# Kernel tuning notes

Hardware: AMD Instinct MI355X
Metric: run time of the kernel (lower is better)

Reference implementation:

```python
import jax, jax.numpy as jnp
import numpy as np

B, S, H = 2, 2048, 4096
NH, NKV, HD = 32, 8, 128
NEG = -1e9


def _rotary(x, cos, sin):
    # x: [b, s, h, hd]; cos/sin: [b, s, hd//2] -> broadcast over heads
    x = x.reshape(*x.shape[:-1], HD // 2, 2)
    x0, x1 = x[..., 0], x[..., 1]
    c = cos[:, :, None, :]
    s = sin[:, :, None, :]
    out = jnp.stack([x0 * c - x1 * s, x0 * s + x1 * c], axis=-1)
    return out.reshape(*out.shape[:-2], HD)


def setup_inputs() -> dict:
    key = jax.random.key(0)
    ks = jax.random.split(key, 7)
    x = jax.random.normal(ks[0], (B, S, H), dtype=jnp.float32)
    # rotary angles: standard llama freqs
    inv = 1.0 / (10000.0 ** (np.arange(0, HD, 2, dtype=np.float32) / HD))
    t = np.arange(S, dtype=np.float32)
    ang = np.outer(t, inv)  # [S, HD//2]
    freqs_cos = jnp.broadcast_to(jnp.asarray(np.cos(ang)), (B, S, HD // 2))
    freqs_sin = jnp.broadcast_to(jnp.asarray(np.sin(ang)), (B, S, HD // 2))
    sc = 0.02
    wq = jax.random.normal(ks[1], (NH * HD, H), dtype=jnp.float32) * sc
    wk = jax.random.normal(ks[2], (NKV * HD, H), dtype=jnp.float32) * sc
    wv = jax.random.normal(ks[3], (NKV * HD, H), dtype=jnp.float32) * sc
    wo = jax.random.normal(ks[4], (H, NH * HD), dtype=jnp.float32) * sc
    return {"x": x, "freqs_cos": freqs_cos, "freqs_sin": freqs_sin,
            "wq": wq, "wk": wk, "wv": wv, "wo": wo}


def reference(x, freqs_cos, freqs_sin, wq, wk, wv, wo):
    b, s, _ = x.shape
    xq = (x @ wq.T).reshape(b, s, NH, HD)
    xk = (x @ wk.T).reshape(b, s, NKV, HD)
    xv = (x @ wv.T).reshape(b, s, NKV, HD)
    xq = _rotary(xq, freqs_cos, freqs_sin)
    xk = _rotary(xk, freqs_cos, freqs_sin)
    # -> [b, heads, s, hd]
    xq = xq.transpose(0, 2, 1, 3)
    xk = xk.transpose(0, 2, 1, 3)
    xv = xv.transpose(0, 2, 1, 3)
    # prefill cache.update returns the freshly written keys/values
    n_rep = NH // NKV
    keys = jnp.repeat(xk, n_rep, axis=1)    # repeat_kv
    values = jnp.repeat(xv, n_rep, axis=1)
    scores = jnp.einsum('bhqd,bhkd->bhqk', xq, keys) / jnp.sqrt(jnp.float32(HD))
    mask = jnp.where(jnp.tril(jnp.ones((s, s), dtype=bool)), 0.0, NEG)
    scores = scores + mask[None, None]
    probs = jax.nn.softmax(scores.astype(jnp.float32), axis=-1).astype(xq.dtype)
    out = jnp.einsum('bhqk,bhkd->bhqd', probs, values)
    out = out.transpose(0, 2, 1, 3).reshape(b, s, NH * HD)
    return out @ wo.T
```

## Files before the change

### kernel.cpp

```cpp
#include <hip/hip_runtime.h>
#include <math.h>

typedef unsigned short u16;
typedef unsigned int u32;
typedef __bf16 bf16x8 __attribute__((ext_vector_type(8)));
typedef float f32x4 __attribute__((ext_vector_type(4)));

#define B_ 2
#define S_ 2048
#define H_ 4096
#define NH_ 32
#define NKV_ 8
#define HD_ 128
#define SCALE 0.08838834764831845f
#define MASK_NEG -30000.0f
#define M_INIT  -1.0e30f

static __device__ __forceinline__ u16 f2bf(float f) {
  union { float f; u32 u; } v; v.f = f;
  u32 u = v.u;
  u += ((u >> 16) & 1u) + 0x7FFFu;
  return (u16)(u >> 16);
}
static __device__ __forceinline__ float bf2f(u16 h) {
  union { u32 u; float f; } v; v.u = ((u32)h) << 16;
  return v.f;
}

template<int F32>
static __device__ __forceinline__ int4 ld8(const void* __restrict__ base, size_t off) {
  if (F32) {
    const float* p = (const float*)base + off;
    const float4 x0 = *(const float4*)p;
    const float4 x1 = *(const float4*)(p + 4);
    union { u16 h[8]; int4 v; } u;
    u.h[0] = f2bf(x0.x); u.h[1] = f2bf(x0.y); u.h[2] = f2bf(x0.z); u.h[3] = f2bf(x0.w);
    u.h[4] = f2bf(x1.x); u.h[5] = f2bf(x1.y); u.h[6] = f2bf(x1.z); u.h[7] = f2bf(x1.w);
    return u.v;
  }
  return *(const int4*)((const u16*)base + off);
}

#define BK 32
#define LDA 40

template<int AF32, int BF32, int OUTF32>
__global__ __launch_bounds__(256) void gemm_bt(const void* __restrict__ A,
                                               const void* __restrict__ Bw,
                                               void* __restrict__ C,
                                               int M, int N, int K) {
  __shared__ u16 As[128 * LDA];
  __shared__ u16 Bs[128 * LDA];
  const int tid  = threadIdx.x;
  const int wave = tid >> 6;
  const int lane = tid & 63;
  const int quad = lane >> 4;
  const int l16  = lane & 15;
  const int wr = wave >> 1, wc = wave & 1;
  const int m0 = blockIdx.y * 128, n0 = blockIdx.x * 128;
  const int srow = tid >> 2;
  const int scol = (tid & 3) << 3;

  f32x4 acc[4][4];
  const f32x4 fz = {0.f, 0.f, 0.f, 0.f};
  for (int i = 0; i < 4; ++i)
    for (int j = 0; j < 4; ++j) acc[i][j] = fz;

  const size_t ao0 = (size_t)(m0 + srow)      * K + scol;
  const size_t ao1 = (size_t)(m0 + srow + 64) * K + scol;
  const size_t bo0 = (size_t)(n0 + srow)      * K + scol;
  const size_t bo1 = (size_t)(n0 + srow + 64) * K + scol;

  for (int k0 = 0; k0 < K; k0 += BK) {
    int4 a0 = ld8<AF32>(A,  ao0 + k0);
    int4 a1 = ld8<AF32>(A,  ao1 + k0);
    int4 b0 = ld8<BF32>(Bw, bo0 + k0);
    int4 b1 = ld8<BF32>(Bw, bo1 + k0);
    __syncthreads();
    *(int4*)&As[srow * LDA + scol]        = a0;
    *(int4*)&As[(srow + 64) * LDA + scol] = a1;
    *(int4*)&Bs[srow * LDA + scol]        = b0;
    *(int4*)&Bs[(srow + 64) * LDA + scol] = b1;
    __syncthreads();
    bf16x8 af[4], bfr[4];
#pragma unroll
    for (int mt = 0; mt < 4; ++mt)
      af[mt] = *(const bf16x8*)&As[(wr * 64 + mt * 16 + l16) * LDA + quad * 8];
#pragma unroll
    for (int nt = 0; nt < 4; ++nt)
      bfr[nt] = *(const bf16x8*)&Bs[(wc * 64 + nt * 16 + l16) * LDA + quad * 8];
#pragma unroll
    for (int mt = 0; mt < 4; ++mt)
#pragma unroll
      for (int nt = 0; nt < 4; ++nt)
        acc[mt][nt] = __builtin_amdgcn_mfma_f32_16x16x32_bf16(af[mt], bfr[nt],
                                                              acc[mt][nt], 0, 0, 0);
  }
#pragma unroll
  for (int mt = 0; mt < 4; ++mt)
#pragma unroll
    for (int nt = 0; nt < 4; ++nt) {
      int row = m0 + wr * 64 + mt * 16 + quad * 4;
      int col = n0 + wc * 64 + nt * 16 + l16;
      if (OUTF32) {
        float* cp = (float*)C + (size_t)row * N + col;
#pragma unroll
        for (int r = 0; r < 4; ++r)
          cp[(size_t)r * N] = acc[mt][nt][r];
      } else {
        u16* cp = (u16*)C + (size_t)row * N + col;
#pragma unroll
        for (int r = 0; r < 4; ++r)
          cp[(size_t)r * N] = f2bf(acc[mt][nt][r]);
      }
    }
}

__global__ __launch_bounds__(256) void cvt_bf16(const float* __restrict__ in,
                                                u16* __restrict__ out, u32 n4) {
  u32 i = blockIdx.x * 256u + threadIdx.x;
  if (i >= n4) return;
  const float4 x = ((const float4*)in)[i];
  u32 lo = (u32)f2bf(x.x) | ((u32)f2bf(x.y) << 16);
  u32 hi = (u32)f2bf(x.z) | ((u32)f2bf(x.w) << 16);
  ((uint2*)out)[i] = make_uint2(lo, hi);
}

#define GLOAD16(gp, lp)                                            \
  __builtin_amdgcn_global_load_lds(                                \
      (__attribute__((address_space(1))) void*)(gp),               \
      (__attribute__((address_space(3))) void*)(lp), 16, 0, 0)

template<int OUTF32>
__global__ __launch_bounds__(256) void gemm_lds(const u16* __restrict__ A,
                                                const u16* __restrict__ Bw,
                                                void* __restrict__ C,
                                                int M, int N, int K) {
  __shared__ u16 As[128 * 32];
  __shared__ u16 Bs[128 * 32];
  const int tid  = threadIdx.x;
  const int wave = tid >> 6;
  const int lane = tid & 63;
  const int quad = lane >> 4;
  const int l16  = lane & 15;
  const int wr = wave >> 1, wc = wave & 1;
  const int m0 = blockIdx.y * 128, n0 = blockIdx.x * 128;

  const int r0 = tid >> 2;
  const int e0 = (tid & 3) << 3;
  const u16* a0 = A  + (size_t)(m0 + r0)      * K + e0;
  const u16* a1 = A  + (size_t)(m0 + r0 + 64) * K + e0;
  const u16* b0 = Bw + (size_t)(n0 + r0)      * K + e0;
  const u16* b1 = Bw + (size_t)(n0 + r0 + 64) * K + e0;
  u16* as0 = As + wave * 512;
  u16* as1 = As + 2048 + wave * 512;
  u16* bs0 = Bs + wave * 512;
  u16* bs1 = Bs + 2048 + wave * 512;

  f32x4 acc[4][4];
  const f32x4 fz = {0.f, 0.f, 0.f, 0.f};
#pragma unroll
  for (int i = 0; i < 4; ++i)
#pragma unroll
    for (int j = 0; j < 4; ++j) acc[i][j] = fz;

  for (int k0 = 0; k0 < K; k0 += 32) {
    __syncthreads();
    GLOAD16(a0 + k0, as0);
    GLOAD16(a1 + k0, as1);
    GLOAD16(b0 + k0, bs0);
    GLOAD16(b1 + k0, bs1);
    __syncthreads();
    bf16x8 af[4], bfr[4];
#pragma unroll
    for (int mt = 0; mt < 4; ++mt)
      af[mt] = *(const bf16x8*)&As[(wr * 64 + mt * 16 + l16) * 32 + quad * 8];
#pragma unroll
    for (int nt = 0; nt < 4; ++nt)
      bfr[nt] = *(const bf16x8*)&Bs[(wc * 64 + nt * 16 + l16) * 32 + quad * 8];
#pragma unroll
    for (int mt = 0; mt < 4; ++mt)
#pragma unroll
      for (int nt = 0; nt < 4; ++nt)
        acc[mt][nt] = __builtin_amdgcn_mfma_f32_16x16x32_bf16(af[mt], bfr[nt],
                                                              acc[mt][nt], 0, 0, 0);
  }
#pragma unroll
  for (int mt = 0; mt < 4; ++mt)
#pragma unroll
    for (int nt = 0; nt < 4; ++nt) {
      int row = m0 + wr * 64 + mt * 16 + quad * 4;
      int col = n0 + wc * 64 + nt * 16 + l16;
      if (OUTF32) {
        float* cp = (float*)C + (size_t)row * N + col;
#pragma unroll
        for (int r = 0; r < 4; ++r)
          cp[(size_t)r * N] = acc[mt][nt][r];
      } else {
        u16* cp = (u16*)C + (size_t)row * N + col;
#pragma unroll
        for (int r = 0; r < 4; ++r)
          cp[(size_t)r * N] = f2bf(acc[mt][nt][r]);
      }
    }
}

__global__ __launch_bounds__(256) void rope_k(u16* __restrict__ Q, u16* __restrict__ Kr,
                                              const float* __restrict__ fc,
                                              const float* __restrict__ fs,
                                              u32 f_bstride) {
  const u32 NQ = (u32)B_ * S_ * NH_ * (HD_ / 2);
  u32 gid = blockIdx.x * 256u + threadIdx.x;
  u16* p;
  u32 b, s, i;
  if (gid < NQ) {
    i = gid & 63u;
    u32 h = (gid >> 6) & 31u;
    s = (gid >> 11) & 2047u;
    b = gid >> 22;
    p = Q + ((size_t)(b * S_ + s) * (NH_ * HD_) + h * HD_ + i * 2);
  } else {
    u32 g = gid - NQ;
    i = g & 63u;
    u32 h = (g >> 6) & 7u;
    s = (g >> 9) & 2047u;
    b = g >> 20;
    p = Kr + ((size_t)(b * S_ + s) * (NKV_ * HD_) + h * HD_ + i * 2);
  }
  u32 xx = *(const u32*)p;
  float x0 = bf2f((u16)(xx & 0xffffu));
  float x1 = bf2f((u16)(xx >> 16));
  u32 fidx = b * f_bstride + s * (HD_ / 2) + i;
  float c  = fc[fidx];
  float sn = fs[fidx];
  float o0 = x0 * c - x1 * sn;
  float o1 = x0 * sn + x1 * c;
  *(u32*)p = (u32)f2bf(o0) | ((u32)f2bf(o1) << 16);
}

__global__ __launch_bounds__(256) void attn_k(const u16* Q,
                                              const u16* __restrict__ Kr,
                                              const u16* __restrict__ V,
                                              u16* O) {
  __shared__ u16 Ks[64 * 136];
  __shared__ u16 Vs[128 * 72];
  __shared__ u16 Ps[64 * 72];
  const int tid  = threadIdx.x;
  const int wave = tid >> 6;
  const int lane = tid & 63;
  const int quad = lane >> 4;
  const int l16  = lane & 15;
  const int qt = blockIdx.x;
  const int h  = blockIdx.y;
  const int b  = blockIdx.z;
  const int kvh = h >> 2;
  const int q0  = qt * 64;

  const u16* Qb = Q  + (size_t)b * S_ * (NH_ * HD_)  + (size_t)h * HD_;
  const u16* Kb = Kr + (size_t)b * S_ * (NKV_ * HD_) + (size_t)kvh * HD_;
  const u16* Vb = V  + (size_t)b * S_ * (NKV_ * HD_) + (size_t)kvh * HD_;

  bf16x8 qf[4];
  {
    const u16* qrow = Qb + (size_t)(q0 + wave * 16 + l16) * (NH_ * HD_);
#pragma unroll
    for (int ks = 0; ks < 4; ++ks)
      qf[ks] = *(const bf16x8*)&qrow[ks * 32 + quad * 8];
  }

  float m_run[4] = {M_INIT, M_INIT, M_INIT, M_INIT};
  float l_run[4] = {0.f, 0.f, 0.f, 0.f};
  f32x4 o_acc[8];
  const f32x4 fz = {0.f, 0.f, 0.f, 0.f};
#pragma unroll
  for (int dt = 0; dt < 8; ++dt) o_acc[dt] = fz;

  const int lr = tid >> 4;
  const int lc = (tid & 15) << 3;

  for (int j = 0; j <= qt; ++j) {
    __syncthreads();
#pragma unroll
    for (int p = 0; p < 4; ++p) {
      int row = p * 16 + lr;
      size_t goff = (size_t)(j * 64 + row) * (NKV_ * HD_) + lc;
      int4 kv4 = *(const int4*)(Kb + goff);
      int4 vv4 = *(const int4*)(Vb + goff);
      *(int4*)&Ks[row * 136 + lc] = kv4;
      u16* vp = (u16*)&vv4;
#pragma unroll
      for (int i = 0; i < 8; ++i) Vs[(lc + i) * 72 + row] = vp[i];
    }
    __syncthreads();

    f32x4 s[4];
#pragma unroll
    for (int nt = 0; nt < 4; ++nt) {
      f32x4 a = fz;
#pragma unroll
      for (int ks = 0; ks < 4; ++ks) {
        bf16x8 kf = *(const bf16x8*)&Ks[(nt * 16 + l16) * 136 + ks * 32 + quad * 8];
        a = __builtin_amdgcn_mfma_f32_16x16x32_bf16(qf[ks], kf, a, 0, 0, 0);
      }
#pragma unroll
      for (int r = 0; r < 4; ++r) a[r] *= SCALE;
      s[nt] = a;
    }
    if (j == qt) {
#pragma unroll
      for (int nt = 0; nt < 4; ++nt)
#pragma unroll
        for (int r = 0; r < 4; ++r) {
          int col = nt * 16 + l16;
          int rw  = wave * 16 + quad * 4 + r;
          if (col > rw) s[nt][r] = MASK_NEG;
        }
    }

    float alpha[4], mnew[4];
#pragma unroll
    for (int r = 0; r < 4; ++r) {
      float v = fmaxf(fmaxf(s[0][r], s[1][r]), fmaxf(s[2][r], s[3][r]));
      v = fmaxf(v, __shfl_xor(v, 1));
      v = fmaxf(v, __shfl_xor(v, 2));
      v = fmaxf(v, __shfl_xor(v, 4));
      v = fmaxf(v, __shfl_xor(v, 8));
      mnew[r]  = fmaxf(m_run[r], v);
      alpha[r] = __expf(m_run[r] - mnew[r]);
      m_run[r] = mnew[r];
    }
    float rs[4] = {0.f, 0.f, 0.f, 0.f};
#pragma unroll
    for (int nt = 0; nt < 4; ++nt)
#pragma unroll
      for (int r = 0; r < 4; ++r) {
        float pv = __expf(s[nt][r] - mnew[r]);
        rs[r] += pv;
        Ps[(wave * 16 + quad * 4 + r) * 72 + nt * 16 + l16] = f2bf(pv);
      }
#pragma unroll
    for (int r = 0; r < 4; ++r) {
      float v = rs[r];
      v += __shfl_xor(v, 1);
      v += __shfl_xor(v, 2);
      v += __shfl_xor(v, 4);
      v += __shfl_xor(v, 8);
      l_run[r] = l_run[r] * alpha[r] + v;
    }
#pragma unroll
    for (int dt = 0; dt < 8; ++dt)
#pragma unroll
      for (int r = 0; r < 4; ++r) o_acc[dt][r] *= alpha[r];
    __syncthreads();

#pragma unroll
    for (int ks2 = 0; ks2 < 2; ++ks2) {
      bf16x8 pf = *(const bf16x8*)&Ps[(wave * 16 + l16) * 72 + ks2 * 32 + quad * 8];
#pragma unroll
      for (int dt = 0; dt < 8; ++dt) {
        bf16x8 vf = *(const bf16x8*)&Vs[(dt * 16 + l16) * 72 + ks2 * 32 + quad * 8];
        o_acc[dt] = __builtin_amdgcn_mfma_f32_16x16x32_bf16(pf, vf, o_acc[dt], 0, 0, 0);
      }
    }
  }

#pragma unroll
  for (int r = 0; r < 4; ++r) {
    float inv = 1.f / l_run[r];
    int srow = q0 + wave * 16 + quad * 4 + r;
    u16* op = O + (size_t)(b * S_ + srow) * (NH_ * HD_) + h * HD_ + l16;
#pragma unroll
    for (int dt = 0; dt < 8; ++dt)
      op[dt * 16] = f2bf(o_acc[dt][r] * inv);
  }
}

extern "C" void kernel_launch(void* const* d_in, const int* in_sizes, int n_in,
                              void* d_out, int out_size, void* d_ws, size_t ws_size,
                              hipStream_t stream) {
  (void)n_in; (void)out_size;
  const void*  x  = d_in[0];
  const float* fc = (const float*)d_in[1];
  const float* fs = (const float*)d_in[2];
  const void*  wq = d_in[3];
  const void*  wk = d_in[4];
  const void*  wv = d_in[5];
  const void*  wo = d_in[6];

  u16* Qraw = (u16*)d_ws;
  u16* Kraw = Qraw + (size_t)B_ * S_ * NH_ * HD_;
  u16* Vraw = Kraw + (size_t)B_ * S_ * NKV_ * HD_;

  u32 f_bstride = (in_sizes[1] >= (int)(B_ * S_ * (HD_ / 2))) ? (u32)(S_ * (HD_ / 2)) : 0u;

  const size_t elems_x = (size_t)B_ * S_ * H_;
  const size_t need = ((size_t)B_ * S_ * (NH_ + 2 * NKV_) * HD_ + 2 * elems_x) * 2;

  if (ws_size >= need) {
    u16* Xbf = Vraw + (size_t)B_ * S_ * NKV_ * HD_;
    u16* Wbf = Xbf + elems_x;
    cvt_bf16<<<16384, 256, 0, stream>>>((const float*)x, Xbf, 4194304u);
    cvt_bf16<<<16384, 256, 0, stream>>>((const float*)wq, Wbf, 4194304u);
    gemm_lds<0><<<dim3(32, 32), 256, 0, stream>>>(Xbf, Wbf, Qraw, 4096, 4096, 4096);
    cvt_bf16<<<4096, 256, 0, stream>>>((const float*)wk, Wbf, 1048576u);
    gemm_lds<0><<<dim3(8, 32), 256, 0, stream>>>(Xbf, Wbf, Kraw, 4096, 1024, 4096);
    cvt_bf16<<<4096, 256, 0, stream>>>((const float*)wv, Wbf, 1048576u);
    gemm_lds<0><<<dim3(8, 32), 256, 0, stream>>>(Xbf, Wbf, Vraw, 4096, 1024, 4096);
    rope_k<<<40960, 256, 0, stream>>>(Qraw, Kraw, fc, fs, f_bstride);
    attn_k<<<dim3(32, 32, 2), 256, 0, stream>>>(Qraw, Kraw, Vraw,  Qraw);
    cvt_bf16<<<16384, 256, 0, stream>>>((const float*)wo, Wbf, 4194304u);
    gemm_lds<1><<<dim3(32, 32), 256, 0, stream>>>(Qraw, Wbf, d_out, 4096, 4096, 4096);
  } else {
    gemm_bt<1, 1, 0><<<dim3(32, 32), 256, 0, stream>>>(x, wq, Qraw, 4096, 4096, 4096);
    gemm_bt<1, 1, 0><<<dim3(8, 32),  256, 0, stream>>>(x, wk, Kraw, 4096, 1024, 4096);
    gemm_bt<1, 1, 0><<<dim3(8, 32),  256, 0, stream>>>(x, wv, Vraw, 4096, 1024, 4096);
    rope_k<<<40960, 256, 0, stream>>>(Qraw, Kraw, fc, fs, f_bstride);
    attn_k<<<dim3(32, 32, 2), 256, 0, stream>>>(Qraw, Kraw, Vraw, Qraw);
    gemm_bt<0, 1, 1><<<dim3(32, 32), 256, 0, stream>>>(Qraw, wo, d_out, 4096, 4096, 4096);
  }
}
```

Measured before the change: 1.498 ms.

## Prefetch K/V to registers, use transpose LDS reads for V, transpose score layout

Restructures the attention inner loop. The next K/V tile is loaded into registers while the current tile is computed. V is stored to LDS with vector writes in a swizzled layout and read back with ds_read_b64_tr_b16, replacing the scalar transposing stores. The QK^T MFMA operands are swapped so each lane holds one query row, which makes the softmax max and sum reductions cheaper and allows packed P stores. It also removes one __syncthreads per iteration, adds s_setprio hints and sets launch bounds to 3 blocks per CU. The cost is higher register pressure from the prefetch buffers, and the layout math has to stay consistent with the transpose-read semantics.

```diff
diff --git a/kernel.cpp b/kernel.cpp
--- a/kernel.cpp
+++ b/kernel.cpp
@@ -5,6 +5,7 @@
 typedef unsigned int u32;
 typedef __bf16 bf16x8 __attribute__((ext_vector_type(8)));
 typedef float f32x4 __attribute__((ext_vector_type(4)));
+typedef unsigned int u32x2 __attribute__((ext_vector_type(2)));
 
 #define B_ 2
 #define S_ 2048
@@ -238,12 +239,21 @@
   *(u32*)p = (u32)f2bf(o0) | ((u32)f2bf(o1) << 16);
 }
 
-__global__ __launch_bounds__(256) void attn_k(const u16* Q,
-                                              const u16* __restrict__ Kr,
-                                              const u16* __restrict__ V,
-                                              u16* O) {
+template<int IMM>
+static __device__ __forceinline__ u32x2 trread(const u16* p) {
+  u32x2 d;
+  asm volatile("ds_read_b64_tr_b16 %0, %1 offset:%2"
+               : "=v"(d)
+               : "v"((__attribute__((address_space(3))) const u16*)p), "n"(IMM));
+  return d;
+}
+
+__global__ __launch_bounds__(256, 3) void attn_k(const u16* Q,
+                                                 const u16* __restrict__ Kr,
+                                                 const u16* __restrict__ V,
+                                                 u16* O) {
   __shared__ u16 Ks[64 * 136];
-  __shared__ u16 Vs[128 * 72];
+  __shared__ u16 Vsub[8192];
   __shared__ u16 Ps[64 * 72];
   const int tid  = threadIdx.x;
   const int wave = tid >> 6;
@@ -268,8 +278,8 @@
       qf[ks] = *(const bf16x8*)&qrow[ks * 32 + quad * 8];
   }
 
-  float m_run[4] = {M_INIT, M_INIT, M_INIT, M_INIT};
-  float l_run[4] = {0.f, 0.f, 0.f, 0.f};
+  float m_run = M_INIT;
+  float l_run = 0.f;
   f32x4 o_acc[8];
   const f32x4 fz = {0.f, 0.f, 0.f, 0.f};
 #pragma unroll
@@ -277,96 +287,133 @@
 
   const int lr = tid >> 4;
   const int lc = (tid & 15) << 3;
+  const u16* vb = &Vsub[quad * 1024 + l16 * 4];
+
+  int4 kreg[4], vreg[4];
+#pragma unroll
+  for (int p = 0; p < 4; ++p) {
+    size_t g = (size_t)(p * 16 + lr) * (NKV_ * HD_) + lc;
+    kreg[p] = *(const int4*)(Kb + g);
+    vreg[p] = *(const int4*)(Vb + g);
+  }
 
   for (int j = 0; j <= qt; ++j) {
     __syncthreads();
 #pragma unroll
     for (int p = 0; p < 4; ++p) {
-      int row = p * 16 + lr;
-      size_t goff = (size_t)(j * 64 + row) * (NKV_ * HD_) + lc;
-      int4 kv4 = *(const int4*)(Kb + goff);
-      int4 vv4 = *(const int4*)(Vb + goff);
-      *(int4*)&Ks[row * 136 + lc] = kv4;
-      u16* vp = (u16*)&vv4;
-#pragma unroll
-      for (int i = 0; i < 8; ++i) Vs[(lc + i) * 72 + row] = vp[i];
-    }
-    __syncthreads();
+      int kv = p * 16 + lr;
+      *(int4*)&Ks[kv * 136 + lc] = kreg[p];
+      *(int4*)&Vsub[((kv >> 2) * 8 + (lc >> 4)) * 64 + (kv & 3) * 16 + (lc & 8)] = vreg[p];
+    }
+    __syncthreads();
+    if (j < qt) {
+#pragma unroll
+      for (int p = 0; p < 4; ++p) {
+        size_t g = (size_t)((j + 1) * 64 + p * 16 + lr) * (NKV_ * HD_) + lc;
+        kreg[p] = *(const int4*)(Kb + g);
+        vreg[p] = *(const int4*)(Vb + g);
+      }
+    }
 
     f32x4 s[4];
+    __builtin_amdgcn_s_setprio(1);
 #pragma unroll
     for (int nt = 0; nt < 4; ++nt) {
       f32x4 a = fz;
 #pragma unroll
       for (int ks = 0; ks < 4; ++ks) {
         bf16x8 kf = *(const bf16x8*)&Ks[(nt * 16 + l16) * 136 + ks * 32 + quad * 8];
-        a = __builtin_amdgcn_mfma_f32_16x16x32_bf16(qf[ks], kf, a, 0, 0, 0);
+        a = __builtin_amdgcn_mfma_f32_16x16x32_bf16(kf, qf[ks], a, 0, 0, 0);
       }
 #pragma unroll
       for (int r = 0; r < 4; ++r) a[r] *= SCALE;
       s[nt] = a;
     }
+    __builtin_amdgcn_s_setprio(0);
     if (j == qt) {
 #pragma unroll
       for (int nt = 0; nt < 4; ++nt)
 #pragma unroll
-        for (int r = 0; r < 4; ++r) {
-          int col = nt * 16 + l16;
-          int rw  = wave * 16 + quad * 4 + r;
-          if (col > rw) s[nt][r] = MASK_NEG;
+        for (int r = 0; r < 4; ++r)
+          if (nt * 16 + quad * 4 + r > wave * 16 + l16) s[nt][r] = MASK_NEG;
+    }
+
+    float pmax;
+    {
+      float x0 = fmaxf(fmaxf(s[0][0], s[0][1]), fmaxf(s[0][2], s[0][3]));
+      float x1 = fmaxf(fmaxf(s[1][0], s[1][1]), fmaxf(s[1][2], s[1][3]));
+      float x2 = fmaxf(fmaxf(s[2][0], s[2][1]), fmaxf(s[2][2], s[2][3]));
+      float x3 = fmaxf(fmaxf(s[3][0], s[3][1]), fmaxf(s[3][2], s[3][3]));
+      pmax = fmaxf(fmaxf(x0, x1), fmaxf(x2, x3));
+      pmax = fmaxf(pmax, __shfl_xor(pmax, 16));
+      pmax = fmaxf(pmax, __shfl_xor(pmax, 32));
+    }
+    float mnew  = fmaxf(m_run, pmax);
+    float alpha = __expf(m_run - mnew);
+    m_run = mnew;
+
+    float rs = 0.f;
+#pragma unroll
+    for (int nt = 0; nt < 4; ++nt) {
+      float p0 = __expf(s[nt][0] - mnew);
+      float p1 = __expf(s[nt][1] - mnew);
+      float p2 = __expf(s[nt][2] - mnew);
+      float p3 = __expf(s[nt][3] - mnew);
+      rs += (p0 + p1) + (p2 + p3);
+      u32 w0 = (u32)f2bf(p0) | ((u32)f2bf(p1) << 16);
+      u32 w1 = (u32)f2bf(p2) | ((u32)f2bf(p3) << 16);
+      *(uint2*)&Ps[(wave * 16 + l16) * 72 + nt * 16 + quad * 4] = make_uint2(w0, w1);
+    }
+    asm volatile("" ::: "memory");
+    rs += __shfl_xor(rs, 16);
+    rs += __shfl_xor(rs, 32);
+    l_run = l_run * alpha + rs;
+
+    float a4[4];
+#pragma unroll
+    for (int r = 0; r < 4; ++r) a4[r] = __shfl(alpha, quad * 4 + r);
+#pragma unroll
+    for (int dt = 0; dt < 8; ++dt)
+#pragma unroll
+      for (int r = 0; r < 4; ++r) o_acc[dt][r] *= a4[r];
+
+#pragma unroll
+    for (int ks2 = 0; ks2 < 2; ++ks2) {
+      bf16x8 pa = *(const bf16x8*)&Ps[(wave * 16 + l16) * 72 + ks2 * 32 + quad * 8];
+      u32x2 t[8][2];
+      if (ks2 == 0) {
+#pragma unroll
+        for (int dt = 0; dt < 8; ++dt) {
+          const u16* vp = vb + dt * 64;
+          t[dt][0] = trread<0>(vp);
+          t[dt][1] = trread<1024>(vp);
         }
-    }
-
-    float alpha[4], mnew[4];
-#pragma unroll
-    for (int r = 0; r < 4; ++r) {
-      float v = fmaxf(fmaxf(s[0][r], s[1][r]), fmaxf(s[2][r], s[3][r]));
-      v = fmaxf(v, __shfl_xor(v, 1));
-      v = fmaxf(v, __shfl_xor(v, 2));
-      v = fmaxf(v, __shfl_xor(v, 4));
-      v = fmaxf(v, __shfl_xor(v, 8));
-      mnew[r]  = fmaxf(m_run[r], v);
-      alpha[r] = __expf(m_run[r] - mnew[r]);
-      m_run[r] = mnew[r];
-    }
-    float rs[4] = {0.f, 0.f, 0.f, 0.f};
-#pragma unroll
-    for (int nt = 0; nt < 4; ++nt)
-#pragma unroll
-      for (int r = 0; r < 4; ++r) {
-        float pv = __expf(s[nt][r] - mnew[r]);
-        rs[r] += pv;
-        Ps[(wave * 16 + quad * 4 + r) * 72 + nt * 16 + l16] = f2bf(pv);
-      }
-#pragma unroll
-    for (int r = 0; r < 4; ++r) {
-      float v = rs[r];
-      v += __shfl_xor(v, 1);
-      v += __shfl_xor(v, 2);
-      v += __shfl_xor(v, 4);
-      v += __shfl_xor(v, 8);
-      l_run[r] = l_run[r] * alpha[r] + v;
-    }
-#pragma unroll
-    for (int dt = 0; dt < 8; ++dt)
-#pragma unroll
-      for (int r = 0; r < 4; ++r) o_acc[dt][r] *= alpha[r];
-    __syncthreads();
-
-#pragma unroll
-    for (int ks2 = 0; ks2 < 2; ++ks2) {
-      bf16x8 pf = *(const bf16x8*)&Ps[(wave * 16 + l16) * 72 + ks2 * 32 + quad * 8];
+      } else {
+#pragma unroll
+        for (int dt = 0; dt < 8; ++dt) {
+          const u16* vp = vb + dt * 64;
+          t[dt][0] = trread<8192>(vp);
+          t[dt][1] = trread<8192 + 1024>(vp);
+        }
+      }
+      asm volatile("s_waitcnt lgkmcnt(0)" ::: "memory");
+      __builtin_amdgcn_sched_barrier(0);
+      __builtin_amdgcn_s_setprio(1);
 #pragma unroll
       for (int dt = 0; dt < 8; ++dt) {
-        bf16x8 vf = *(const bf16x8*)&Vs[(dt * 16 + l16) * 72 + ks2 * 32 + quad * 8];
-        o_acc[dt] = __builtin_amdgcn_mfma_f32_16x16x32_bf16(pf, vf, o_acc[dt], 0, 0, 0);
-      }
+        union { u32 w[4]; bf16x8 v; } uf;
+        uf.w[0] = t[dt][0][0]; uf.w[1] = t[dt][0][1];
+        uf.w[2] = t[dt][1][0]; uf.w[3] = t[dt][1][1];
+        o_acc[dt] = __builtin_amdgcn_mfma_f32_16x16x32_bf16(pa, uf.v, o_acc[dt], 0, 0, 0);
+      }
+      __builtin_amdgcn_s_setprio(0);
     }
   }
 
 #pragma unroll
   for (int r = 0; r < 4; ++r) {
-    float inv = 1.f / l_run[r];
+    float lv  = __shfl(l_run, quad * 4 + r);
+    float inv = 1.f / lv;
     int srow = q0 + wave * 16 + quad * 4 + r;
     u16* op = O + (size_t)(b * S_ + srow) * (NH_ * HD_) + h * HD_ + l16;
 #pragma unroll
```

Result: faster. 1.347 ms (-10.1%).
